# Optimization experiments

Hardware: AMD Instinct MI355X
Metric: run time of the kernel (lower is better)

The kernel has to match this reference:

```python
import jax, jax.numpy as jnp
import numpy as np

LAYERS = 20
STACKS = 2
LPS = LAYERS // STACKS  # layers per stack -> dilations 2**(l % LPS)
OUT_CH = 256
RES_CH = 64
GATE_CH = 128
SKIP_CH = 256


def setup_inputs() -> dict:
    key = jax.random.key(0)
    ks = jax.random.split(key, 16)
    B, T = 8, 16000
    s = 0.05
    inp = {
        "x": jax.random.normal(ks[0], (B, OUT_CH, T), dtype=jnp.float32),
        # first causal conv (note: original code applies w_pre to the shifted
        # input twice -> output is 2*w_pre(pre); w_cur is unused, so omitted)
        "w_pre0": jax.random.normal(ks[1], (RES_CH, OUT_CH)) * s,
        "b_pre0": jax.random.normal(ks[2], (RES_CH,)) * s,
        # per-layer dilated conv (no bias), residual block, skip projection
        "w_dil_pre": jax.random.normal(ks[3], (LAYERS, GATE_CH, RES_CH)) * s,
        "w_dil_cur": jax.random.normal(ks[4], (LAYERS, GATE_CH, RES_CH)) * s,
        "bias_h": jax.random.normal(ks[5], (LAYERS, GATE_CH)) * s,
        "w_res": jax.random.normal(ks[6], (LAYERS, RES_CH, RES_CH)) * s,
        "b_res": jax.random.normal(ks[7], (LAYERS, RES_CH)) * s,
        "w_skip": jax.random.normal(ks[8], (LAYERS, SKIP_CH, RES_CH)) * s,
        "b_skip": jax.random.normal(ks[9], (LAYERS, SKIP_CH)) * s,
        # output head
        "w_relu": jax.random.normal(ks[10], (SKIP_CH, SKIP_CH)) * s,
        "b_relu": jax.random.normal(ks[11], (SKIP_CH,)) * s,
        "w_out": jax.random.normal(ks[12], (OUT_CH, SKIP_CH)) * s,
        "b_out": jax.random.normal(ks[13], (OUT_CH,)) * s,
    }
    return inp


def _shift_right(h, d):
    # causal shift: pad d zeros on the left along time, drop last d samples
    return jnp.pad(h, ((0, 0), (0, 0), (d, 0)))[:, :, :-d]


def reference(x, w_pre0, b_pre0, w_dil_pre, w_dil_cur, bias_h,
              w_res, b_res, w_skip, b_skip, w_relu, b_relu, w_out, b_out):
    # first causal conv: original Conv2X1 'casual' path computes
    # w_pre(pre) + w_pre(pre) = 2 * w_pre(pre)  (faithful to source)
    pre = _shift_right(x, 1)
    h = 2.0 * (jnp.einsum('rc,bct->brt', w_pre0, pre) + b_pre0[None, :, None])

    skip = jnp.zeros((x.shape[0], SKIP_CH, x.shape[2]), dtype=h.dtype)
    for l in range(LAYERS):
        d = 2 ** (l % LPS)
        h_pre = _shift_right(h, d)
        # dilated 2x1 conv = two channel-wise linears (no bias), summed with bias_h
        a = (jnp.einsum('gr,brt->bgt', w_dil_pre[l], h_pre)
             + jnp.einsum('gr,brt->bgt', w_dil_cur[l], h)
             + bias_h[l][None, :, None])
        g = jnp.tanh(a[:, :RES_CH]) * jax.nn.sigmoid(a[:, RES_CH:])
        res = jnp.einsum('rq,bqt->brt', w_res[l], g) + b_res[l][None, :, None]
        h = h + res
        skip = skip + jnp.einsum('sr,brt->bst', w_skip[l], g) + b_skip[l][None, :, None]

    o = jax.nn.relu(skip)
    o = jnp.einsum('ps,bst->bpt', w_relu, o) + b_relu[None, :, None]
    o = jax.nn.relu(o)
    logits = jnp.einsum('os,bst->bot', w_out, o) + b_out[None, :, None]
    return jax.nn.softmax(logits, axis=1)  # (B, out_channels, T)
```

## Files before the change

kernel.cpp:

```cpp
#include <hip/hip_runtime.h>
#include <math.h>

#define B_ 8
#define T_ 16000
#define NBT 250
#define HROWS 16512
#define NLAY 20

typedef __attribute__((ext_vector_type(8))) short bf16x8;
typedef __attribute__((ext_vector_type(4))) float f32x4;
typedef __attribute__((ext_vector_type(4))) short sh4;

__device__ __forceinline__ unsigned short f2bf(float f){
  unsigned u = __float_as_uint(f);
  u += 0x7fffu + ((u >> 16) & 1u);
  return (unsigned short)(u >> 16);
}
__device__ __forceinline__ float bf2f(unsigned short s){
  return __uint_as_float(((unsigned)s) << 16);
}
__device__ __forceinline__ void split2(float v, unsigned short& hi, unsigned short& lo){
  hi = f2bf(v);
  lo = f2bf(v - bf2f(hi));
}

#define MFMA(a,b,c) __builtin_amdgcn_mfma_f32_16x16x32_bf16((a),(b),(c),0,0,0)

__device__ __forceinline__ void gload16(const short* gsrc, short* ldst){
  __builtin_amdgcn_global_load_lds(
      (const __attribute__((address_space(1))) unsigned int*)gsrc,
      (__attribute__((address_space(3))) unsigned int*)ldst, 16, 0, 0);
}

__global__ void k_split(const float* __restrict__ src, short* __restrict__ hi,
                        short* __restrict__ lo, int n){
  int idx = blockIdx.x * 256 + threadIdx.x;
  if (idx < n){
    unsigned short h, l; split2(src[idx], h, l);
    hi[idx] = (short)h; lo[idx] = (short)l;
  }
}
__global__ void k_split_gate(const float* __restrict__ wdp, const float* __restrict__ wdc,
                             short* __restrict__ hi, short* __restrict__ lo){
  int idx = blockIdx.x * 256 + threadIdx.x;
  if (idx < NLAY*128*128){
    int l   = idx >> 14;
    int rem = idx & 16383;
    int row = rem >> 7;
    int k   = rem & 127;
    float v = (k < 64) ? wdp[(l*128 + row)*64 + k] : wdc[(l*128 + row)*64 + (k-64)];
    unsigned short h, lo16; split2(v, h, lo16);
    hi[idx] = (short)h; lo[idx] = (short)lo16;
  }
}
__global__ void k_pack_wsf(const float* __restrict__ wsk, short* __restrict__ wsf){
  int idx = blockIdx.x * 256 + threadIdx.x;
  if (idx < NLAY*8*2*2*64*8){
    int e    = idx & 7;
    int j    = (idx >> 3) & 63;
    int kb2  = (idx >> 9) & 1;
    int half = (idx >> 10) & 1;
    int w    = (idx >> 11) & 7;
    int l    = idx >> 14;
    int row  = w*32 + half*16 + (j & 15);
    int ch   = (kb2*4 + (j >> 4))*8 + e;
    wsf[idx] = (short)f2bf(wsk[((size_t)l*256 + row)*64 + ch]);
  }
}
__global__ void k_bsum(const float* __restrict__ bsk, float* __restrict__ bsum){
  int s = threadIdx.x;
  if (s < 256){
    float a = 0.f;
#pragma unroll
    for (int l = 0; l < NLAY; ++l) a += bsk[l*256 + s];
    bsum[s] = a;
  }
}
__global__ void k_zero_guard(short* __restrict__ hA, short* __restrict__ hB){
  int idx = blockIdx.x * 256 + threadIdx.x;
  if (idx < B_*512*128){
    int b = idx / (512*128);
    int rem = idx - b*(512*128);
    size_t off = (size_t)b*HROWS*128 + rem;
    hA[off] = 0; hB[off] = 0;
  }
}

__global__ __launch_bounds__(512) void k_head_in(
    const float* __restrict__ x, const short* __restrict__ wph,
    const short* __restrict__ wpl, const float* __restrict__ bias,
    short* __restrict__ h)
{
  __shared__ short SXh[64*256], SXl[64*256];
  const int tid = threadIdx.x;
  const int bb = blockIdx.x / NBT;
  const int t0 = (blockIdx.x % NBT) * 64;
  const int lane = tid & 63, w = tid >> 6;
  const int l16 = lane & 15, l4 = lane >> 4;

  const float* xb = x + (size_t)bb * 256 * T_;
  {
    int col = lane;
    int t = t0 + col - 1;
#pragma unroll
    for (int p = 0; p < 16; ++p){
      int k0 = w*32 + p*2;
      float v0 = (t >= 0) ? xb[(size_t)k0*T_ + t] : 0.f;
      float v1 = (t >= 0) ? xb[(size_t)(k0+1)*T_ + t] : 0.f;
      unsigned short h0,l0,h1,l1; split2(v0,h0,l0); split2(v1,h1,l1);
      int idx = col*256 + (k0 ^ ((col & 15) << 3));
      ((unsigned int*)SXh)[idx>>1] = (unsigned)h0 | ((unsigned)h1 << 16);
      ((unsigned int*)SXl)[idx>>1] = (unsigned)l0 | ((unsigned)l1 << 16);
    }
  }
  __syncthreads();

  const int mi = w & 3, nh = w >> 2;
  const int rowA = mi*16 + l16;
  const int rt0 = mi*16 + l4*4;
  bf16x8 Ah[8], Al[8];
#pragma unroll
  for (int kb = 0; kb < 8; ++kb){
    int ko = kb*32 + l4*8;
    Ah[kb] = *(const bf16x8*)(wph + (size_t)rowA*256 + ko);
    Al[kb] = *(const bf16x8*)(wpl + (size_t)rowA*256 + ko);
  }
  short* hb = h + ((size_t)bb*HROWS + 512)*128;
#pragma unroll
  for (int nt = 0; nt < 2; ++nt){
    int col = (nh*2 + nt)*16 + l16;
    f32x4 acc = {0.f,0.f,0.f,0.f};
#pragma unroll
    for (int kb = 0; kb < 8; ++kb){
      int ko = (kb*32 + l4*8) ^ (l16 << 3);
      bf16x8 bhv = *(const bf16x8*)&SXh[col*256 + ko];
      bf16x8 blv = *(const bf16x8*)&SXl[col*256 + ko];
      acc = MFMA(Ah[kb], bhv, acc);
      acc = MFMA(Ah[kb], blv, acc);
      acc = MFMA(Al[kb], bhv, acc);
    }
    int t = t0 + col;
    int key = t & 15;
    int c  = rt0 >> 3, sub = rt0 & 7;
    sh4 hv, lv;
#pragma unroll
    for (int r = 0; r < 4; ++r){
      float v = 2.f*(acc[r] + bias[rt0 + r]);
      unsigned short hh, ll; split2(v, hh, ll);
      hv[r] = (short)hh; lv[r] = (short)ll;
    }
    *(sh4*)&hb[(size_t)t*128 + ((c ^ key) << 3) + sub] = hv;
    *(sh4*)&hb[(size_t)t*128 + (((c + 8) ^ key) << 3) + sub] = lv;
  }
}

__global__ __launch_bounds__(512) void k_layer4(
    const short* __restrict__ hin, short* __restrict__ hout,
    short* __restrict__ gout,
    const short* __restrict__ wgh, const short* __restrict__ wgl,
    const short* __restrict__ wrh, const short* __restrict__ wrlo,
    const float* __restrict__ bh, const float* __restrict__ br, int d)
{
  __shared__ short SH[64*128];
  __shared__ short SHP[64*128];
  __shared__ short SGh[64*64], SGl[64*64];
  const int tid = threadIdx.x;
  const int bb = blockIdx.x / NBT;
  const int tile = blockIdx.x % NBT;
  const int t0 = tile * 64;
  const int lane = tid & 63, w = tid >> 6;
  const int l16 = lane & 15, l4 = lane >> 4;

  const short* hb = hin + ((size_t)bb*HROWS + 512)*128;
  {
#pragma unroll
    for (int i = 0; i < 2; ++i){
      int colb = (w*2 + i)*4;
      const short* s1 = hb + (size_t)(t0 + colb + (lane>>4))*128 + (lane&15)*8;
      gload16(s1, &SH[colb*128]);
      const short* s2 = hb + (size_t)(t0 - d + colb + (lane>>4))*128 + (lane&15)*8;
      gload16(s2, &SHP[colb*128]);
    }
  }

  const int mi = w & 3, nh = w >> 2;
  const int rt0 = mi*16 + l4*4;
  const int rowt = mi*16 + l16, rows = 64 + mi*16 + l16;
  bf16x8 Ath[4], Atl[4], Ash[4], Asl[4];
#pragma unroll
  for (int kb = 0; kb < 4; ++kb){
    int ko = kb*32 + l4*8;
    Ath[kb] = *(const bf16x8*)(wgh + (size_t)rowt*128 + ko);
    Atl[kb] = *(const bf16x8*)(wgl + (size_t)rowt*128 + ko);
    Ash[kb] = *(const bf16x8*)(wgh + (size_t)rows*128 + ko);
    Asl[kb] = *(const bf16x8*)(wgl + (size_t)rows*128 + ko);
  }
  float bt[4], bs[4];
#pragma unroll
  for (int r = 0; r < 4; ++r){ bt[r] = bh[rt0+r]; bs[r] = bh[64+rt0+r]; }
  __syncthreads();

#pragma unroll
  for (int nt = 0; nt < 2; ++nt){
    int col = (nh*2 + nt)*16 + l16;
    int keyC = col & 15;
    int keyP = (col - d) & 15;
    f32x4 at = {0.f,0.f,0.f,0.f}, as = {0.f,0.f,0.f,0.f};
#pragma unroll
    for (int kb = 0; kb < 4; ++kb){
      const short* tile_p = (kb < 2) ? SHP : SH;
      int key = (kb < 2) ? keyP : keyC;
      int cb = (kb & 1)*4 + l4;
      bf16x8 bhv = *(const bf16x8*)&tile_p[col*128 + ((cb ^ key) << 3)];
      bf16x8 blv = *(const bf16x8*)&tile_p[col*128 + (((cb + 8) ^ key) << 3)];
      at = MFMA(Ath[kb], bhv, at);
      at = MFMA(Ath[kb], blv, at);
      at = MFMA(Atl[kb], bhv, at);
      as = MFMA(Ash[kb], bhv, as);
      as = MFMA(Ash[kb], blv, as);
      as = MFMA(Asl[kb], bhv, as);
    }
    unsigned short gh4[4], gl4[4];
#pragma unroll
    for (int r = 0; r < 4; ++r){
      float av = at[r] + bt[r];
      float sv = as[r] + bs[r];
      float e2 = __expf(2.f*av);
      float tv = 1.f - 2.f/(e2 + 1.f);
      float sg = 1.f/(1.f + __expf(-sv));
      float g  = tv*sg;
      split2(g, gh4[r], gl4[r]);
      int gi = col*64 + ((rt0 + r) ^ ((col & 7) << 3));
      SGh[gi] = (short)gh4[r]; SGl[gi] = (short)gl4[r];
    }
  }
  __syncthreads();

  {
    int f = tid >> 6, j = tid & 63;
    int row = (f >> 1)*16 + (j & 15);
    int c   = (f & 1)*4 + (j >> 4);
    bf16x8 v = *(const bf16x8*)&SGh[row*64 + ((c ^ (row & 7)) << 3)];
    *(bf16x8*)(gout + ((size_t)bb*NBT + tile)*4096 + tid*8) = v;
  }

  {
    const int rowA = mi*16 + l16;
    bf16x8 Rh[2], Rl[2];
#pragma unroll
    for (int kb = 0; kb < 2; ++kb){
      int ko = kb*32 + l4*8;
      Rh[kb] = *(const bf16x8*)(wrh  + (size_t)rowA*64 + ko);
      Rl[kb] = *(const bf16x8*)(wrlo + (size_t)rowA*64 + ko);
    }
    short* ho = hout + ((size_t)bb*HROWS + 512)*128;
    const int cH = rt0 >> 3, sub = rt0 & 7;
#pragma unroll
    for (int nt = 0; nt < 2; ++nt){
      int col = (nh*2 + nt)*16 + l16;
      int keyC = col & 15;
      f32x4 acc = {0.f,0.f,0.f,0.f};
#pragma unroll
      for (int kb = 0; kb < 2; ++kb){
        int ko = (kb*32 + l4*8) ^ ((col & 7) << 3);
        bf16x8 bhv = *(const bf16x8*)&SGh[col*64 + ko];
        bf16x8 blv = *(const bf16x8*)&SGl[col*64 + ko];
        acc = MFMA(Rh[kb], bhv, acc);
        acc = MFMA(Rh[kb], blv, acc);
        acc = MFMA(Rl[kb], bhv, acc);
      }
      sh4 hi4 = *(const sh4*)&SH[col*128 + ((cH ^ keyC) << 3) + sub];
      sh4 lo4 = *(const sh4*)&SH[col*128 + (((cH + 8) ^ keyC) << 3) + sub];
      int t = t0 + col;
      sh4 hv, lv;
#pragma unroll
      for (int r = 0; r < 4; ++r){
        float hin_f = bf2f((unsigned short)hi4[r]) + bf2f((unsigned short)lo4[r]);
        float v = hin_f + acc[r] + br[rt0 + r];
        unsigned short hh, ll; split2(v, hh, ll);
        hv[r] = (short)hh; lv[r] = (short)ll;
      }
      *(sh4*)&ho[(size_t)t*128 + ((cH ^ keyC) << 3) + sub] = hv;
      *(sh4*)&ho[(size_t)t*128 + (((cH + 8) ^ keyC) << 3) + sub] = lv;
    }
  }
}

__global__ __launch_bounds__(512) void k_head_fused(
    float* __restrict__ io,
    const short* __restrict__ g,
    const short* __restrict__ wsf,
    const float* __restrict__ bsum,
    const short* __restrict__ wrlh, const short* __restrict__ wrll,
    const float* __restrict__ brl,
    const short* __restrict__ woh, const short* __restrict__ wol,
    const float* __restrict__ bo)
{
  __shared__ short GT[2][64*64];
  __shared__ short S1h[64*256];
  const int tid = threadIdx.x;
  const int bb = blockIdx.x / NBT;
  const int tile = blockIdx.x % NBT;
  const int t0 = tile * 64;
  const int lane = tid & 63, w = tid >> 6;
  const int l16 = lane & 15, l4 = lane >> 4;

  const int r0 = w*32 + l16, r1 = w*32 + 16 + l16;
  const int rtb0 = w*32 + l4*4, rtb1 = rtb0 + 16;

  f32x4 acc0[4], acc1[4];
#pragma unroll
  for (int nt = 0; nt < 4; ++nt){ acc0[nt] = (f32x4){0.f,0.f,0.f,0.f}; acc1[nt] = (f32x4){0.f,0.f,0.f,0.f}; }

  {
    const size_t LSTR = (size_t)B_ * NBT * 4096;
    const short* gtile = g + ((size_t)bb*NBT + tile)*4096;
    const short* wb = wsf + (size_t)w*2048 + lane*8;

#define STAGE(l20, buf) gload16(gtile + (size_t)(l20)*LSTR + w*512 + lane*8, &GT[buf][w*512])

    STAGE(0, 0);
    for (int l20 = 0; l20 < 20; ++l20){
      if (l20 + 1 < 20){
        STAGE(l20 + 1, (l20 + 1) & 1);
        asm volatile("s_waitcnt vmcnt(1)" ::: "memory");
      } else {
        asm volatile("s_waitcnt vmcnt(0)" ::: "memory");
      }
      __builtin_amdgcn_s_barrier();
      __builtin_amdgcn_sched_barrier(0);
      const short* wl = wb + (size_t)l20*16384;
      bf16x8 A00 = *(const bf16x8*)(wl);
      bf16x8 A01 = *(const bf16x8*)(wl + 512);
      bf16x8 A10 = *(const bf16x8*)(wl + 1024);
      bf16x8 A11 = *(const bf16x8*)(wl + 1536);
      const short* gt = &GT[l20 & 1][0];
#pragma unroll
      for (int nt = 0; nt < 4; ++nt){
        bf16x8 B0 = *(const bf16x8*)(gt + (nt*2    )*512 + lane*8);
        bf16x8 B1 = *(const bf16x8*)(gt + (nt*2 + 1)*512 + lane*8);
        acc0[nt] = MFMA(A00, B0, acc0[nt]);
        acc0[nt] = MFMA(A01, B1, acc0[nt]);
        acc1[nt] = MFMA(A10, B0, acc1[nt]);
        acc1[nt] = MFMA(A11, B1, acc1[nt]);
      }
      __builtin_amdgcn_sched_barrier(0);
      __builtin_amdgcn_s_barrier();
    }
#undef STAGE
  }

  {
    float bs0[4], bs1[4];
#pragma unroll
    for (int r = 0; r < 4; ++r){ bs0[r] = bsum[rtb0+r]; bs1[r] = bsum[rtb1+r]; }
#pragma unroll
    for (int nt = 0; nt < 4; ++nt){
      int c2 = nt*16 + l16;
      unsigned short h[4];
#pragma unroll
      for (int r = 0; r < 4; ++r)
        h[r] = f2bf(fmaxf(acc0[nt][r] + bs0[r], 0.f));
      int i0 = c2*256 + (rtb0 ^ (l16 << 3));
      ((unsigned int*)&S1h[i0])[0] = (unsigned)h[0] | ((unsigned)h[1] << 16);
      ((unsigned int*)&S1h[i0])[1] = (unsigned)h[2] | ((unsigned)h[3] << 16);
#pragma unroll
      for (int r = 0; r < 4; ++r)
        h[r] = f2bf(fmaxf(acc1[nt][r] + bs1[r], 0.f));
      int i1 = c2*256 + (rtb1 ^ (l16 << 3));
      ((unsigned int*)&S1h[i1])[0] = (unsigned)h[0] | ((unsigned)h[1] << 16);
      ((unsigned int*)&S1h[i1])[1] = (unsigned)h[2] | ((unsigned)h[3] << 16);
    }
  }
  __syncthreads();

#pragma unroll
  for (int nt = 0; nt < 4; ++nt){ acc0[nt] = (f32x4){0.f,0.f,0.f,0.f}; acc1[nt] = (f32x4){0.f,0.f,0.f,0.f}; }
#pragma unroll
  for (int kb = 0; kb < 8; ++kb){
    int ko = kb*32 + l4*8;
    bf16x8 A0h = *(const bf16x8*)(wrlh + (size_t)r0*256 + ko);
    bf16x8 A0l = *(const bf16x8*)(wrll + (size_t)r0*256 + ko);
    bf16x8 A1h = *(const bf16x8*)(wrlh + (size_t)r1*256 + ko);
    bf16x8 A1l = *(const bf16x8*)(wrll + (size_t)r1*256 + ko);
#pragma unroll
    for (int nt = 0; nt < 4; ++nt){
      int c2 = nt*16 + l16;
      int kos = ko ^ (l16 << 3);
      bf16x8 bhv = *(const bf16x8*)&S1h[c2*256 + kos];
      acc0[nt] = MFMA(A0h, bhv, acc0[nt]);
      acc0[nt] = MFMA(A0l, bhv, acc0[nt]);
      acc1[nt] = MFMA(A1h, bhv, acc1[nt]);
      acc1[nt] = MFMA(A1l, bhv, acc1[nt]);
    }
  }
  __syncthreads();
  {
    float br0[4], br1[4];
#pragma unroll
    for (int r = 0; r < 4; ++r){ br0[r] = brl[rtb0+r]; br1[r] = brl[rtb1+r]; }
#pragma unroll
    for (int nt = 0; nt < 4; ++nt){
      int c2 = nt*16 + l16;
      unsigned short h[4];
#pragma unroll
      for (int r = 0; r < 4; ++r)
        h[r] = f2bf(fmaxf(acc0[nt][r] + br0[r], 0.f));
      int i0 = c2*256 + (rtb0 ^ (l16 << 3));
      ((unsigned int*)&S1h[i0])[0] = (unsigned)h[0] | ((unsigned)h[1] << 16);
      ((unsigned int*)&S1h[i0])[1] = (unsigned)h[2] | ((unsigned)h[3] << 16);
#pragma unroll
      for (int r = 0; r < 4; ++r)
        h[r] = f2bf(fmaxf(acc1[nt][r] + br1[r], 0.f));
      int i1 = c2*256 + (rtb1 ^ (l16 << 3));
      ((unsigned int*)&S1h[i1])[0] = (unsigned)h[0] | ((unsigned)h[1] << 16);
      ((unsigned int*)&S1h[i1])[1] = (unsigned)h[2] | ((unsigned)h[3] << 16);
    }
  }
  __syncthreads();

#pragma unroll
  for (int nt = 0; nt < 4; ++nt){ acc0[nt] = (f32x4){0.f,0.f,0.f,0.f}; acc1[nt] = (f32x4){0.f,0.f,0.f,0.f}; }
#pragma unroll
  for (int kb = 0; kb < 8; ++kb){
    int ko = kb*32 + l4*8;
    bf16x8 A0h = *(const bf16x8*)(woh + (size_t)r0*256 + ko);
    bf16x8 A0l = *(const bf16x8*)(wol + (size_t)r0*256 + ko);
    bf16x8 A1h = *(const bf16x8*)(woh + (size_t)r1*256 + ko);
    bf16x8 A1l = *(const bf16x8*)(wol + (size_t)r1*256 + ko);
#pragma unroll
    for (int nt = 0; nt < 4; ++nt){
      int c2 = nt*16 + l16;
      int kos = ko ^ (l16 << 3);
      bf16x8 bhv = *(const bf16x8*)&S1h[c2*256 + kos];
      acc0[nt] = MFMA(A0h, bhv, acc0[nt]);
      acc0[nt] = MFMA(A0l, bhv, acc0[nt]);
      acc1[nt] = MFMA(A1h, bhv, acc1[nt]);
      acc1[nt] = MFMA(A1l, bhv, acc1[nt]);
    }
  }
  float* smax = (float*)&GT[0][0];
  float* ssum = smax + 512;
  float* iob = io + (size_t)bb * 256 * T_;
  float bo0[4], bo1[4];
#pragma unroll
  for (int r = 0; r < 4; ++r){ bo0[r] = bo[rtb0+r]; bo1[r] = bo[rtb1+r]; }
#pragma unroll
  for (int nt = 0; nt < 4; ++nt){
    float m = -1e30f;
#pragma unroll
    for (int r = 0; r < 4; ++r){
      acc0[nt][r] += bo0[r];
      acc1[nt][r] += bo1[r];
      m = fmaxf(m, fmaxf(acc0[nt][r], acc1[nt][r]));
    }
    m = fmaxf(m, __shfl_xor(m, 16, 64));
    m = fmaxf(m, __shfl_xor(m, 32, 64));
    smax[w*64 + nt*16 + l16] = m;
  }
  __syncthreads();
#pragma unroll
  for (int nt = 0; nt < 4; ++nt){
    float m = smax[nt*16 + l16];
#pragma unroll
    for (int ww = 1; ww < 8; ++ww) m = fmaxf(m, smax[ww*64 + nt*16 + l16]);
    float s = 0.f;
#pragma unroll
    for (int r = 0; r < 4; ++r){
      acc0[nt][r] = __expf(acc0[nt][r] - m); s += acc0[nt][r];
      acc1[nt][r] = __expf(acc1[nt][r] - m); s += acc1[nt][r];
    }
    s += __shfl_xor(s, 16, 64);
    s += __shfl_xor(s, 32, 64);
    ssum[w*64 + nt*16 + l16] = s;
  }
  __syncthreads();
#pragma unroll
  for (int nt = 0; nt < 4; ++nt){
    float S = 0.f;
#pragma unroll
    for (int ww = 0; ww < 8; ++ww) S += ssum[ww*64 + nt*16 + l16];
    float inv = 1.f / S;
    int t = t0 + nt*16 + l16;
#pragma unroll
    for (int r = 0; r < 4; ++r){
      iob[(size_t)(rtb0 + r)*T_ + t] = acc0[nt][r]*inv;
      iob[(size_t)(rtb1 + r)*T_ + t] = acc1[nt][r]*inv;
    }
  }
}

extern "C" void kernel_launch(void* const* d_in, const int* in_sizes, int n_in,
                              void* d_out, int out_size, void* d_ws, size_t ws_size,
                              hipStream_t stream) {
  const float* x       = (const float*)d_in[0];
  const float* w_pre0  = (const float*)d_in[1];
  const float* b_pre0  = (const float*)d_in[2];
  const float* w_dil_p = (const float*)d_in[3];
  const float* w_dil_c = (const float*)d_in[4];
  const float* bias_h  = (const float*)d_in[5];
  const float* w_res   = (const float*)d_in[6];
  const float* b_res   = (const float*)d_in[7];
  const float* w_skip  = (const float*)d_in[8];
  const float* b_skip  = (const float*)d_in[9];
  const float* w_relu  = (const float*)d_in[10];
  const float* b_relu  = (const float*)d_in[11];
  const float* w_out   = (const float*)d_in[12];
  const float* b_out   = (const float*)d_in[13];

  float* out = (float*)d_out;
  short* hA = (short*)d_ws;
  short* hB = hA + (size_t)B_ * HROWS * 128;
  float* bsum = (float*)(hB + (size_t)B_ * HROWS * 128);
  short* p   = (short*)(bsum + 256);
  short* WPh = p; p += 16384;  short* WPl = p; p += 16384;
  short* WGh = p; p += 327680; short* WGl = p; p += 327680;
  short* WRh = p; p += 81920;  short* WRl = p; p += 81920;
  short* WSF = p; p += 327680;
  short* WLh = p; p += 65536;  short* WLl = p; p += 65536;
  short* WOh = p; p += 65536;  short* WOl = p; p += 65536;
  short* GBUF = p;

  k_split<<<64, 256, 0, stream>>>(w_pre0, WPh, WPl, 16384);
  k_split_gate<<<1280, 256, 0, stream>>>(w_dil_p, w_dil_c, WGh, WGl);
  k_split<<<320, 256, 0, stream>>>(w_res, WRh, WRl, 81920);
  k_pack_wsf<<<1280, 256, 0, stream>>>(w_skip, WSF);
  k_split<<<256, 256, 0, stream>>>(w_relu, WLh, WLl, 65536);
  k_split<<<256, 256, 0, stream>>>(w_out, WOh, WOl, 65536);
  k_zero_guard<<<2048, 256, 0, stream>>>(hA, hB);
  k_bsum<<<1, 256, 0, stream>>>(b_skip, bsum);

  k_head_in<<<B_ * NBT, 512, 0, stream>>>(x, WPh, WPl, b_pre0, hA);

  const short* hin = hA;
  short* houtp = hB;
  for (int l = 0; l < NLAY; ++l) {
    int d = 1 << (l % 10);
    k_layer4<<<B_ * NBT, 512, 0, stream>>>(
        hin, houtp,
        GBUF + (size_t)l * B_ * NBT * 4096,
        WGh + (size_t)l*16384, WGl + (size_t)l*16384,
        WRh + (size_t)l*4096,  WRl + (size_t)l*4096,
        bias_h + (size_t)l*128, b_res + (size_t)l*64, d);
    const short* tmp = hin;
    hin = houtp;
    houtp = (short*)tmp;
  }

  k_head_fused<<<B_ * NBT, 512, 0, stream>>>(
      out, GBUF, WSF, bsum, WLh, WLl, b_relu, WOh, WOl, b_out);
}
```

Before: 1.333 ms.

## Make layer kernel persistent over four tiles with double-buffered prefetch

The per-layer kernel now processes four consecutive time tiles per block, loading the gate and residual weights once and double-buffering the next tile's current and shifted h rows into LDS while the current tile computes. The separate shifted tile is merged into one 128-row window, reusing overlapping rows when the dilation is below 64. The head kernel aliases its LDS buffers into one pool and issues the skip-weight loads before the barrier. The aims are lower weight-reload and load-latency cost and higher occupancy, at the price of four times fewer blocks and extra barriers.

```diff
diff --git a/kernel.cpp b/kernel.cpp
--- a/kernel.cpp
+++ b/kernel.cpp
@@ -154,37 +154,23 @@
   }
 }
 
-__global__ __launch_bounds__(512) void k_layer4(
+__global__ __launch_bounds__(512, 4) void k_layer5(
     const short* __restrict__ hin, short* __restrict__ hout,
     short* __restrict__ gout,
     const short* __restrict__ wgh, const short* __restrict__ wgl,
     const short* __restrict__ wrh, const short* __restrict__ wrlo,
     const float* __restrict__ bh, const float* __restrict__ br, int d)
 {
-  __shared__ short SH[64*128];
-  __shared__ short SHP[64*128];
+  __shared__ short SHX[2][128*128];
   __shared__ short SGh[64*64], SGl[64*64];
   const int tid = threadIdx.x;
-  const int bb = blockIdx.x / NBT;
-  const int tile = blockIdx.x % NBT;
-  const int t0 = tile * 64;
   const int lane = tid & 63, w = tid >> 6;
   const int l16 = lane & 15, l4 = lane >> 4;
-
-  const short* hb = hin + ((size_t)bb*HROWS + 512)*128;
-  {
-#pragma unroll
-    for (int i = 0; i < 2; ++i){
-      int colb = (w*2 + i)*4;
-      const short* s1 = hb + (size_t)(t0 + colb + (lane>>4))*128 + (lane&15)*8;
-      gload16(s1, &SH[colb*128]);
-      const short* s2 = hb + (size_t)(t0 - d + colb + (lane>>4))*128 + (lane&15)*8;
-      gload16(s2, &SHP[colb*128]);
-    }
-  }
-
   const int mi = w & 3, nh = w >> 2;
   const int rt0 = mi*16 + l4*4;
+  const int dmax = (d > 64) ? d : 64;
+  const int spoff = (d < 64) ? (64 - d) : 0;
+
   const int rowt = mi*16 + l16, rows = 64 + mi*16 + l16;
   bf16x8 Ath[4], Atl[4], Ash[4], Asl[4];
 #pragma unroll
@@ -195,94 +181,130 @@
     Ash[kb] = *(const bf16x8*)(wgh + (size_t)rows*128 + ko);
     Asl[kb] = *(const bf16x8*)(wgl + (size_t)rows*128 + ko);
   }
-  float bt[4], bs[4];
-#pragma unroll
-  for (int r = 0; r < 4; ++r){ bt[r] = bh[rt0+r]; bs[r] = bh[64+rt0+r]; }
-  __syncthreads();
-
-#pragma unroll
-  for (int nt = 0; nt < 2; ++nt){
-    int col = (nh*2 + nt)*16 + l16;
-    int keyC = col & 15;
-    int keyP = (col - d) & 15;
-    f32x4 at = {0.f,0.f,0.f,0.f}, as = {0.f,0.f,0.f,0.f};
-#pragma unroll
-    for (int kb = 0; kb < 4; ++kb){
-      const short* tile_p = (kb < 2) ? SHP : SH;
-      int key = (kb < 2) ? keyP : keyC;
-      int cb = (kb & 1)*4 + l4;
-      bf16x8 bhv = *(const bf16x8*)&tile_p[col*128 + ((cb ^ key) << 3)];
-      bf16x8 blv = *(const bf16x8*)&tile_p[col*128 + (((cb + 8) ^ key) << 3)];
-      at = MFMA(Ath[kb], bhv, at);
-      at = MFMA(Ath[kb], blv, at);
-      at = MFMA(Atl[kb], bhv, at);
-      as = MFMA(Ash[kb], bhv, as);
-      as = MFMA(Ash[kb], blv, as);
-      as = MFMA(Asl[kb], bhv, as);
-    }
-    unsigned short gh4[4], gl4[4];
-#pragma unroll
-    for (int r = 0; r < 4; ++r){
-      float av = at[r] + bt[r];
-      float sv = as[r] + bs[r];
-      float e2 = __expf(2.f*av);
-      float tv = 1.f - 2.f/(e2 + 1.f);
-      float sg = 1.f/(1.f + __expf(-sv));
-      float g  = tv*sg;
-      split2(g, gh4[r], gl4[r]);
-      int gi = col*64 + ((rt0 + r) ^ ((col & 7) << 3));
-      SGh[gi] = (short)gh4[r]; SGl[gi] = (short)gl4[r];
-    }
-  }
-  __syncthreads();
-
-  {
-    int f = tid >> 6, j = tid & 63;
-    int row = (f >> 1)*16 + (j & 15);
-    int c   = (f & 1)*4 + (j >> 4);
-    bf16x8 v = *(const bf16x8*)&SGh[row*64 + ((c ^ (row & 7)) << 3)];
-    *(bf16x8*)(gout + ((size_t)bb*NBT + tile)*4096 + tid*8) = v;
-  }
-
-  {
-    const int rowA = mi*16 + l16;
-    bf16x8 Rh[2], Rl[2];
-#pragma unroll
-    for (int kb = 0; kb < 2; ++kb){
-      int ko = kb*32 + l4*8;
-      Rh[kb] = *(const bf16x8*)(wrh  + (size_t)rowA*64 + ko);
-      Rl[kb] = *(const bf16x8*)(wrlo + (size_t)rowA*64 + ko);
-    }
-    short* ho = hout + ((size_t)bb*HROWS + 512)*128;
-    const int cH = rt0 >> 3, sub = rt0 & 7;
+  bf16x8 Rh[2], Rl[2];
+#pragma unroll
+  for (int kb = 0; kb < 2; ++kb){
+    int ko = kb*32 + l4*8;
+    Rh[kb] = *(const bf16x8*)(wrh  + (size_t)rowt*64 + ko);
+    Rl[kb] = *(const bf16x8*)(wrlo + (size_t)rowt*64 + ko);
+  }
+  float bt[4], bs[4], brv[4];
+#pragma unroll
+  for (int r = 0; r < 4; ++r){
+    bt[r] = bh[rt0+r]; bs[r] = bh[64+rt0+r]; brv[r] = br[rt0+r];
+  }
+
+  const int gt0 = blockIdx.x * 4;
+
+  auto STAGE = [&](int gt, int buf){
+    int bb2 = gt / NBT;
+    int t0s = (gt % NBT) * 64;
+    const short* hb2 = hin + ((size_t)bb2*HROWS + 512)*128;
+#pragma unroll
+    for (int j = 0; j < 4; ++j){
+      int chunk = j >> 1;
+      int rq = (w*2 + (j & 1))*4;
+      int grow = (chunk ? t0s : t0s - dmax) + rq + (lane >> 4);
+      gload16(hb2 + (size_t)grow*128 + (lane & 15)*8,
+              &SHX[buf][(chunk*64 + rq)*128]);
+    }
+  };
+
+  STAGE(gt0, 0);
+  for (int it = 0; it < 4; ++it){
+    const int gt = gt0 + it;
+    const int bb = gt / NBT, tile = gt % NBT;
+    const int t0 = tile * 64;
+    if (it < 3){
+      STAGE(gt + 1, (it + 1) & 1);
+      asm volatile("s_waitcnt vmcnt(4)" ::: "memory");
+    } else {
+      asm volatile("s_waitcnt vmcnt(0)" ::: "memory");
+    }
+    __builtin_amdgcn_s_barrier();
+    __builtin_amdgcn_sched_barrier(0);
+
+    const short* SX = &SHX[it & 1][0];
 #pragma unroll
     for (int nt = 0; nt < 2; ++nt){
       int col = (nh*2 + nt)*16 + l16;
-      int keyC = col & 15;
-      f32x4 acc = {0.f,0.f,0.f,0.f};
-#pragma unroll
-      for (int kb = 0; kb < 2; ++kb){
-        int ko = (kb*32 + l4*8) ^ ((col & 7) << 3);
-        bf16x8 bhv = *(const bf16x8*)&SGh[col*64 + ko];
-        bf16x8 blv = *(const bf16x8*)&SGl[col*64 + ko];
-        acc = MFMA(Rh[kb], bhv, acc);
-        acc = MFMA(Rh[kb], blv, acc);
-        acc = MFMA(Rl[kb], bhv, acc);
+      int keyC = (t0 + col) & 15;
+      int keyP = (t0 + col - d) & 15;
+      f32x4 at = {0.f,0.f,0.f,0.f}, as = {0.f,0.f,0.f,0.f};
+#pragma unroll
+      for (int kb = 0; kb < 4; ++kb){
+        int xr  = (kb < 2) ? (spoff + col) : (64 + col);
+        int key = (kb < 2) ? keyP : keyC;
+        int cb = (kb & 1)*4 + l4;
+        bf16x8 bhv = *(const bf16x8*)&SX[xr*128 + ((cb ^ key) << 3)];
+        bf16x8 blv = *(const bf16x8*)&SX[xr*128 + (((cb + 8) ^ key) << 3)];
+        at = MFMA(Ath[kb], bhv, at);
+        at = MFMA(Ath[kb], blv, at);
+        at = MFMA(Atl[kb], bhv, at);
+        as = MFMA(Ash[kb], bhv, as);
+        as = MFMA(Ash[kb], blv, as);
+        as = MFMA(Asl[kb], bhv, as);
       }
-      sh4 hi4 = *(const sh4*)&SH[col*128 + ((cH ^ keyC) << 3) + sub];
-      sh4 lo4 = *(const sh4*)&SH[col*128 + (((cH + 8) ^ keyC) << 3) + sub];
-      int t = t0 + col;
-      sh4 hv, lv;
+      unsigned short gh4[4], gl4[4];
 #pragma unroll
       for (int r = 0; r < 4; ++r){
-        float hin_f = bf2f((unsigned short)hi4[r]) + bf2f((unsigned short)lo4[r]);
-        float v = hin_f + acc[r] + br[rt0 + r];
-        unsigned short hh, ll; split2(v, hh, ll);
-        hv[r] = (short)hh; lv[r] = (short)ll;
+        float av = at[r] + bt[r];
+        float sv = as[r] + bs[r];
+        float e2 = __expf(2.f*av);
+        float tv = 1.f - 2.f/(e2 + 1.f);
+        float sg = 1.f/(1.f + __expf(-sv));
+        float g  = tv*sg;
+        split2(g, gh4[r], gl4[r]);
+        int gi = col*64 + ((rt0 + r) ^ ((col & 7) << 3));
+        SGh[gi] = (short)gh4[r]; SGl[gi] = (short)gl4[r];
       }
-      *(sh4*)&ho[(size_t)t*128 + ((cH ^ keyC) << 3) + sub] = hv;
-      *(sh4*)&ho[(size_t)t*128 + (((cH + 8) ^ keyC) << 3) + sub] = lv;
-    }
+    }
+    asm volatile("s_waitcnt lgkmcnt(0)" ::: "memory");
+    __builtin_amdgcn_sched_barrier(0);
+    __builtin_amdgcn_s_barrier();
+
+    {
+      int f = tid >> 6, j = tid & 63;
+      int row = (f >> 1)*16 + (j & 15);
+      int c   = (f & 1)*4 + (j >> 4);
+      bf16x8 v = *(const bf16x8*)&SGh[row*64 + ((c ^ (row & 7)) << 3)];
+      *(bf16x8*)(gout + ((size_t)bb*NBT + tile)*4096 + tid*8) = v;
+    }
+
+    {
+      short* ho = hout + ((size_t)bb*HROWS + 512)*128;
+      const int cH = rt0 >> 3, sub = rt0 & 7;
+#pragma unroll
+      for (int nt = 0; nt < 2; ++nt){
+        int col = (nh*2 + nt)*16 + l16;
+        int keyC = (t0 + col) & 15;
+        f32x4 acc = {0.f,0.f,0.f,0.f};
+#pragma unroll
+        for (int kb = 0; kb < 2; ++kb){
+          int ko = (kb*32 + l4*8) ^ ((col & 7) << 3);
+          bf16x8 bhv = *(const bf16x8*)&SGh[col*64 + ko];
+          bf16x8 blv = *(const bf16x8*)&SGl[col*64 + ko];
+          acc = MFMA(Rh[kb], bhv, acc);
+          acc = MFMA(Rh[kb], blv, acc);
+          acc = MFMA(Rl[kb], bhv, acc);
+        }
+        sh4 hi4 = *(const sh4*)&SX[(64 + col)*128 + ((cH ^ keyC) << 3) + sub];
+        sh4 lo4 = *(const sh4*)&SX[(64 + col)*128 + (((cH + 8) ^ keyC) << 3) + sub];
+        int t = t0 + col;
+        sh4 hv, lv;
+#pragma unroll
+        for (int r = 0; r < 4; ++r){
+          float hin_f = bf2f((unsigned short)hi4[r]) + bf2f((unsigned short)lo4[r]);
+          float v = hin_f + acc[r] + brv[r];
+          unsigned short hh, ll; split2(v, hh, ll);
+          hv[r] = (short)hh; lv[r] = (short)ll;
+        }
+        *(sh4*)&ho[(size_t)t*128 + ((cH ^ keyC) << 3) + sub] = hv;
+        *(sh4*)&ho[(size_t)t*128 + (((cH + 8) ^ keyC) << 3) + sub] = lv;
+      }
+    }
+    __builtin_amdgcn_sched_barrier(0);
+    __builtin_amdgcn_s_barrier();
   }
 }
 
@@ -296,8 +318,7 @@
     const short* __restrict__ woh, const short* __restrict__ wol,
     const float* __restrict__ bo)
 {
-  __shared__ short GT[2][64*64];
-  __shared__ short S1h[64*256];
+  __shared__ short POOL[16384];
   const int tid = threadIdx.x;
   const int bb = blockIdx.x / NBT;
   const int tile = blockIdx.x % NBT;
@@ -317,10 +338,15 @@
     const short* gtile = g + ((size_t)bb*NBT + tile)*4096;
     const short* wb = wsf + (size_t)w*2048 + lane*8;
 
-#define STAGE(l20, buf) gload16(gtile + (size_t)(l20)*LSTR + w*512 + lane*8, &GT[buf][w*512])
+#define STAGE(l20, buf) gload16(gtile + (size_t)(l20)*LSTR + w*512 + lane*8, &POOL[(buf)*4096 + w*512])
 
     STAGE(0, 0);
     for (int l20 = 0; l20 < 20; ++l20){
+      const short* wl = wb + (size_t)l20*16384;
+      bf16x8 A00 = *(const bf16x8*)(wl);
+      bf16x8 A01 = *(const bf16x8*)(wl + 512);
+      bf16x8 A10 = *(const bf16x8*)(wl + 1024);
+      bf16x8 A11 = *(const bf16x8*)(wl + 1536);
       if (l20 + 1 < 20){
         STAGE(l20 + 1, (l20 + 1) & 1);
         asm volatile("s_waitcnt vmcnt(1)" ::: "memory");
@@ -329,12 +355,7 @@
       }
       __builtin_amdgcn_s_barrier();
       __builtin_amdgcn_sched_barrier(0);
-      const short* wl = wb + (size_t)l20*16384;
-      bf16x8 A00 = *(const bf16x8*)(wl);
-      bf16x8 A01 = *(const bf16x8*)(wl + 512);
-      bf16x8 A10 = *(const bf16x8*)(wl + 1024);
-      bf16x8 A11 = *(const bf16x8*)(wl + 1536);
-      const short* gt = &GT[l20 & 1][0];
+      const short* gt = &POOL[(l20 & 1)*4096];
 #pragma unroll
       for (int nt = 0; nt < 4; ++nt){
         bf16x8 B0 = *(const bf16x8*)(gt + (nt*2    )*512 + lane*8);
@@ -350,6 +371,7 @@
 #undef STAGE
   }
 
+  short* S1h = POOL;
   {
     float bs0[4], bs1[4];
 #pragma unroll
@@ -439,7 +461,8 @@
       acc1[nt] = MFMA(A1l, bhv, acc1[nt]);
     }
   }
-  float* smax = (float*)&GT[0][0];
+  __syncthreads();
+  float* smax = (float*)POOL;
   float* ssum = smax + 512;
   float* iob = io + (size_t)bb * 256 * T_;
   float bo0[4], bo1[4];
@@ -536,7 +559,7 @@
   short* houtp = hB;
   for (int l = 0; l < NLAY; ++l) {
     int d = 1 << (l % 10);
-    k_layer4<<<B_ * NBT, 512, 0, stream>>>(
+    k_layer5<<<B_ * NBT / 4, 512, 0, stream>>>(
         hin, houtp,
         GBUF + (size_t)l * B_ * NBT * 4096,
         WGh + (size_t)l*16384, WGl + (size_t)l*16384,
```

Measured after the change: 1.982 ms. +48.7%, slower.

## Add small-dilation layer kernel reusing tile rows for shifted input; merge head shared buffers

Applied to the files above, without the earlier changes.

Adds a specialized layer kernel for dilations up to 32. It loads the 64-column h tile once and reads the shifted (pre) rows from the same shared tile, fetching only a small prefix of d columns from global memory. The goal is to cut the duplicate global reads of the shifted input that the generic layer kernel does. Separately, the head kernel folds its shared buffers into one pool to lower LDS use, and issues the per-layer weight loads before the barrier so they overlap the staging wait; this adds an extra __syncthreads.

```diff
diff --git a/kernel.cpp b/kernel.cpp
--- a/kernel.cpp
+++ b/kernel.cpp
@@ -286,6 +286,143 @@
   }
 }
 
+__global__ __launch_bounds__(512) void k_layer_sd(
+    const short* __restrict__ hin, short* __restrict__ hout,
+    short* __restrict__ gout,
+    const short* __restrict__ wgh, const short* __restrict__ wgl,
+    const short* __restrict__ wrh, const short* __restrict__ wrlo,
+    const float* __restrict__ bh, const float* __restrict__ br, int d)
+{
+  __shared__ short SH[64*128];
+  __shared__ short PREF[32*128];
+  __shared__ short SGh[64*64], SGl[64*64];
+  const int tid = threadIdx.x;
+  const int bb = blockIdx.x / NBT;
+  const int tile = blockIdx.x % NBT;
+  const int t0 = tile * 64;
+  const int lane = tid & 63, w = tid >> 6;
+  const int l16 = lane & 15, l4 = lane >> 4;
+
+  const short* hb = hin + ((size_t)bb*HROWS + 512)*128;
+  {
+#pragma unroll
+    for (int i = 0; i < 2; ++i){
+      int colb = (w*2 + i)*4;
+      const short* s1 = hb + (size_t)(t0 + colb + (lane>>4))*128 + (lane&15)*8;
+      gload16(s1, &SH[colb*128]);
+    }
+    if (w*4 < d){
+      const short* s2 = hb + (size_t)(t0 - d + w*4 + (lane>>4))*128 + (lane&15)*8;
+      gload16(s2, &PREF[(w*4)*128]);
+    }
+  }
+
+  const int mi = w & 3, nh = w >> 2;
+  const int rt0 = mi*16 + l4*4;
+  const int rowt = mi*16 + l16, rows = 64 + mi*16 + l16;
+  bf16x8 Ath[4], Atl[4], Ash[4], Asl[4];
+#pragma unroll
+  for (int kb = 0; kb < 4; ++kb){
+    int ko = kb*32 + l4*8;
+    Ath[kb] = *(const bf16x8*)(wgh + (size_t)rowt*128 + ko);
+    Atl[kb] = *(const bf16x8*)(wgl + (size_t)rowt*128 + ko);
+    Ash[kb] = *(const bf16x8*)(wgh + (size_t)rows*128 + ko);
+    Asl[kb] = *(const bf16x8*)(wgl + (size_t)rows*128 + ko);
+  }
+  float bt[4], bs[4];
+#pragma unroll
+  for (int r = 0; r < 4; ++r){ bt[r] = bh[rt0+r]; bs[r] = bh[64+rt0+r]; }
+  __syncthreads();
+
+#pragma unroll
+  for (int nt = 0; nt < 2; ++nt){
+    int col = (nh*2 + nt)*16 + l16;
+    int keyC = col & 15;
+    int keyP = (col - d) & 15;
+    int colp = col - d;
+    const short* prow = (colp >= 0) ? &SH[colp*128] : &PREF[col*128];
+    const short* crow = &SH[col*128];
+    f32x4 at = {0.f,0.f,0.f,0.f}, as = {0.f,0.f,0.f,0.f};
+#pragma unroll
+    for (int kb = 0; kb < 4; ++kb){
+      const short* base = (kb < 2) ? prow : crow;
+      int key = (kb < 2) ? keyP : keyC;
+      int cb = (kb & 1)*4 + l4;
+      bf16x8 bhv = *(const bf16x8*)&base[((cb ^ key) << 3)];
+      bf16x8 blv = *(const bf16x8*)&base[(((cb + 8) ^ key) << 3)];
+      at = MFMA(Ath[kb], bhv, at);
+      at = MFMA(Ath[kb], blv, at);
+      at = MFMA(Atl[kb], bhv, at);
+      as = MFMA(Ash[kb], bhv, as);
+      as = MFMA(Ash[kb], blv, as);
+      as = MFMA(Asl[kb], bhv, as);
+    }
+    unsigned short gh4[4], gl4[4];
+#pragma unroll
+    for (int r = 0; r < 4; ++r){
+      float av = at[r] + bt[r];
+      float sv = as[r] + bs[r];
+      float e2 = __expf(2.f*av);
+      float tv = 1.f - 2.f/(e2 + 1.f);
+      float sg = 1.f/(1.f + __expf(-sv));
+      float g  = tv*sg;
+      split2(g, gh4[r], gl4[r]);
+      int gi = col*64 + ((rt0 + r) ^ ((col & 7) << 3));
+      SGh[gi] = (short)gh4[r]; SGl[gi] = (short)gl4[r];
+    }
+  }
+  __syncthreads();
+
+  {
+    int f = tid >> 6, j = tid & 63;
+    int row = (f >> 1)*16 + (j & 15);
+    int c   = (f & 1)*4 + (j >> 4);
+    bf16x8 v = *(const bf16x8*)&SGh[row*64 + ((c ^ (row & 7)) << 3)];
+    *(bf16x8*)(gout + ((size_t)bb*NBT + tile)*4096 + tid*8) = v;
+  }
+
+  {
+    const int rowA = mi*16 + l16;
+    bf16x8 Rh[2], Rl[2];
+#pragma unroll
+    for (int kb = 0; kb < 2; ++kb){
+      int ko = kb*32 + l4*8;
+      Rh[kb] = *(const bf16x8*)(wrh  + (size_t)rowA*64 + ko);
+      Rl[kb] = *(const bf16x8*)(wrlo + (size_t)rowA*64 + ko);
+    }
+    short* ho = hout + ((size_t)bb*HROWS + 512)*128;
+    const int cH = rt0 >> 3, sub = rt0 & 7;
+#pragma unroll
+    for (int nt = 0; nt < 2; ++nt){
+      int col = (nh*2 + nt)*16 + l16;
+      int keyC = col & 15;
+      f32x4 acc = {0.f,0.f,0.f,0.f};
+#pragma unroll
+      for (int kb = 0; kb < 2; ++kb){
+        int ko = (kb*32 + l4*8) ^ ((col & 7) << 3);
+        bf16x8 bhv = *(const bf16x8*)&SGh[col*64 + ko];
+        bf16x8 blv = *(const bf16x8*)&SGl[col*64 + ko];
+        acc = MFMA(Rh[kb], bhv, acc);
+        acc = MFMA(Rh[kb], blv, acc);
+        acc = MFMA(Rl[kb], bhv, acc);
+      }
+      sh4 hi4 = *(const sh4*)&SH[col*128 + ((cH ^ keyC) << 3) + sub];
+      sh4 lo4 = *(const sh4*)&SH[col*128 + (((cH + 8) ^ keyC) << 3) + sub];
+      int t = t0 + col;
+      sh4 hv, lv;
+#pragma unroll
+      for (int r = 0; r < 4; ++r){
+        float hin_f = bf2f((unsigned short)hi4[r]) + bf2f((unsigned short)lo4[r]);
+        float v = hin_f + acc[r] + br[rt0 + r];
+        unsigned short hh, ll; split2(v, hh, ll);
+        hv[r] = (short)hh; lv[r] = (short)ll;
+      }
+      *(sh4*)&ho[(size_t)t*128 + ((cH ^ keyC) << 3) + sub] = hv;
+      *(sh4*)&ho[(size_t)t*128 + (((cH + 8) ^ keyC) << 3) + sub] = lv;
+    }
+  }
+}
+
 __global__ __launch_bounds__(512) void k_head_fused(
     float* __restrict__ io,
     const short* __restrict__ g,
@@ -296,8 +433,7 @@
     const short* __restrict__ woh, const short* __restrict__ wol,
     const float* __restrict__ bo)
 {
-  __shared__ short GT[2][64*64];
-  __shared__ short S1h[64*256];
+  __shared__ short POOL[16384];
   const int tid = threadIdx.x;
   const int bb = blockIdx.x / NBT;
   const int tile = blockIdx.x % NBT;
@@ -317,10 +453,15 @@
     const short* gtile = g + ((size_t)bb*NBT + tile)*4096;
     const short* wb = wsf + (size_t)w*2048 + lane*8;
 
-#define STAGE(l20, buf) gload16(gtile + (size_t)(l20)*LSTR + w*512 + lane*8, &GT[buf][w*512])
+#define STAGE(l20, buf) gload16(gtile + (size_t)(l20)*LSTR + w*512 + lane*8, &POOL[(buf)*4096 + w*512])
 
     STAGE(0, 0);
     for (int l20 = 0; l20 < 20; ++l20){
+      const short* wl = wb + (size_t)l20*16384;
+      bf16x8 A00 = *(const bf16x8*)(wl);
+      bf16x8 A01 = *(const bf16x8*)(wl + 512);
+      bf16x8 A10 = *(const bf16x8*)(wl + 1024);
+      bf16x8 A11 = *(const bf16x8*)(wl + 1536);
       if (l20 + 1 < 20){
         STAGE(l20 + 1, (l20 + 1) & 1);
         asm volatile("s_waitcnt vmcnt(1)" ::: "memory");
@@ -329,12 +470,7 @@
       }
       __builtin_amdgcn_s_barrier();
       __builtin_amdgcn_sched_barrier(0);
-      const short* wl = wb + (size_t)l20*16384;
-      bf16x8 A00 = *(const bf16x8*)(wl);
-      bf16x8 A01 = *(const bf16x8*)(wl + 512);
-      bf16x8 A10 = *(const bf16x8*)(wl + 1024);
-      bf16x8 A11 = *(const bf16x8*)(wl + 1536);
-      const short* gt = &GT[l20 & 1][0];
+      const short* gt = &POOL[(l20 & 1)*4096];
 #pragma unroll
       for (int nt = 0; nt < 4; ++nt){
         bf16x8 B0 = *(const bf16x8*)(gt + (nt*2    )*512 + lane*8);
@@ -350,6 +486,7 @@
 #undef STAGE
   }
 
+  short* S1h = POOL;
   {
     float bs0[4], bs1[4];
 #pragma unroll
@@ -439,7 +576,8 @@
       acc1[nt] = MFMA(A1l, bhv, acc1[nt]);
     }
   }
-  float* smax = (float*)&GT[0][0];
+  __syncthreads();
+  float* smax = (float*)POOL;
   float* ssum = smax + 512;
   float* iob = io + (size_t)bb * 256 * T_;
   float bo0[4], bo1[4];
@@ -536,12 +674,21 @@
   short* houtp = hB;
   for (int l = 0; l < NLAY; ++l) {
     int d = 1 << (l % 10);
-    k_layer4<<<B_ * NBT, 512, 0, stream>>>(
-        hin, houtp,
-        GBUF + (size_t)l * B_ * NBT * 4096,
-        WGh + (size_t)l*16384, WGl + (size_t)l*16384,
-        WRh + (size_t)l*4096,  WRl + (size_t)l*4096,
-        bias_h + (size_t)l*128, b_res + (size_t)l*64, d);
+    if (d <= 32) {
+      k_layer_sd<<<B_ * NBT, 512, 0, stream>>>(
+          hin, houtp,
+          GBUF + (size_t)l * B_ * NBT * 4096,
+          WGh + (size_t)l*16384, WGl + (size_t)l*16384,
+          WRh + (size_t)l*4096,  WRl + (size_t)l*4096,
+          bias_h + (size_t)l*128, b_res + (size_t)l*64, d);
+    } else {
+      k_layer4<<<B_ * NBT, 512, 0, stream>>>(
+          hin, houtp,
+          GBUF + (size_t)l * B_ * NBT * 4096,
+          WGh + (size_t)l*16384, WGl + (size_t)l*16384,
+          WRh + (size_t)l*4096,  WRl + (size_t)l*4096,
+          bias_h + (size_t)l*128, b_res + (size_t)l*64, d);
+    }
     const short* tmp = hin;
     hin = houtp;
     houtp = (short*)tmp;
```

After: 1.340 ms. About the same (+0.5%).

## Cut LDS and register use in layer and head kernels to raise occupancy

Applied to the files above, without the earlier changes.

The layer kernel drops its separate gate LDS buffers and reuses the previous-tap tile buffer after a barrier. It streams gate weights per k-block instead of keeping all 16 fragments in registers, and sets launch bounds to 6 blocks per CU. The head kernel merges its LDS arrays into one pool, shrinking shared memory from 48KB to 32KB, and issues the skip-weight loads before the stage wait. The aim is more resident blocks per CU to hide latency, at the cost of extra barriers and possible register pressure or spills under the tighter bound.

```diff
diff --git a/kernel.cpp b/kernel.cpp
--- a/kernel.cpp
+++ b/kernel.cpp
@@ -154,7 +154,7 @@
   }
 }
 
-__global__ __launch_bounds__(512) void k_layer4(
+__global__ __launch_bounds__(512, 6) void k_layer6(
     const short* __restrict__ hin, short* __restrict__ hout,
     short* __restrict__ gout,
     const short* __restrict__ wgh, const short* __restrict__ wgl,
@@ -163,7 +163,6 @@
 {
   __shared__ short SH[64*128];
   __shared__ short SHP[64*128];
-  __shared__ short SGh[64*64], SGl[64*64];
   const int tid = threadIdx.x;
   const int bb = blockIdx.x / NBT;
   const int tile = blockIdx.x % NBT;
@@ -186,53 +185,95 @@
   const int mi = w & 3, nh = w >> 2;
   const int rt0 = mi*16 + l4*4;
   const int rowt = mi*16 + l16, rows = 64 + mi*16 + l16;
-  bf16x8 Ath[4], Atl[4], Ash[4], Asl[4];
-#pragma unroll
-  for (int kb = 0; kb < 4; ++kb){
-    int ko = kb*32 + l4*8;
-    Ath[kb] = *(const bf16x8*)(wgh + (size_t)rowt*128 + ko);
-    Atl[kb] = *(const bf16x8*)(wgl + (size_t)rowt*128 + ko);
-    Ash[kb] = *(const bf16x8*)(wgh + (size_t)rows*128 + ko);
-    Asl[kb] = *(const bf16x8*)(wgl + (size_t)rows*128 + ko);
-  }
   float bt[4], bs[4];
 #pragma unroll
   for (int r = 0; r < 4; ++r){ bt[r] = bh[rt0+r]; bs[r] = bh[64+rt0+r]; }
   __syncthreads();
 
+  f32x4 at0 = {0.f,0.f,0.f,0.f}, at1 = {0.f,0.f,0.f,0.f};
+  f32x4 as0 = {0.f,0.f,0.f,0.f}, as1 = {0.f,0.f,0.f,0.f};
+  {
+#pragma unroll
+    for (int kb = 0; kb < 2; ++kb){
+      int ko = kb*32 + l4*8;
+      bf16x8 Wth = *(const bf16x8*)(wgh + (size_t)rowt*128 + ko);
+      bf16x8 Wtl = *(const bf16x8*)(wgl + (size_t)rowt*128 + ko);
+      bf16x8 Wsh = *(const bf16x8*)(wgh + (size_t)rows*128 + ko);
+      bf16x8 Wsl = *(const bf16x8*)(wgl + (size_t)rows*128 + ko);
+      int cb = kb*4 + l4;
+#pragma unroll
+      for (int nt = 0; nt < 2; ++nt){
+        int col = (nh*2 + nt)*16 + l16;
+        int keyP = (col - d) & 15;
+        bf16x8 bhv = *(const bf16x8*)&SHP[col*128 + ((cb ^ keyP) << 3)];
+        bf16x8 blv = *(const bf16x8*)&SHP[col*128 + (((cb + 8) ^ keyP) << 3)];
+        if (nt == 0){
+          at0 = MFMA(Wth, bhv, at0); at0 = MFMA(Wth, blv, at0); at0 = MFMA(Wtl, bhv, at0);
+          as0 = MFMA(Wsh, bhv, as0); as0 = MFMA(Wsh, blv, as0); as0 = MFMA(Wsl, bhv, as0);
+        } else {
+          at1 = MFMA(Wth, bhv, at1); at1 = MFMA(Wth, blv, at1); at1 = MFMA(Wtl, bhv, at1);
+          as1 = MFMA(Wsh, bhv, as1); as1 = MFMA(Wsh, blv, as1); as1 = MFMA(Wsl, bhv, as1);
+        }
+      }
+    }
+  }
+  {
+#pragma unroll
+    for (int kb = 2; kb < 4; ++kb){
+      int ko = kb*32 + l4*8;
+      bf16x8 Wth = *(const bf16x8*)(wgh + (size_t)rowt*128 + ko);
+      bf16x8 Wtl = *(const bf16x8*)(wgl + (size_t)rowt*128 + ko);
+      bf16x8 Wsh = *(const bf16x8*)(wgh + (size_t)rows*128 + ko);
+      bf16x8 Wsl = *(const bf16x8*)(wgl + (size_t)rows*128 + ko);
+      int cb = (kb & 1)*4 + l4;
+#pragma unroll
+      for (int nt = 0; nt < 2; ++nt){
+        int col = (nh*2 + nt)*16 + l16;
+        int keyC = col & 15;
+        bf16x8 bhv = *(const bf16x8*)&SH[col*128 + ((cb ^ keyC) << 3)];
+        bf16x8 blv = *(const bf16x8*)&SH[col*128 + (((cb + 8) ^ keyC) << 3)];
+        if (nt == 0){
+          at0 = MFMA(Wth, bhv, at0); at0 = MFMA(Wth, blv, at0); at0 = MFMA(Wtl, bhv, at0);
+          as0 = MFMA(Wsh, bhv, as0); as0 = MFMA(Wsh, blv, as0); as0 = MFMA(Wsl, bhv, as0);
+        } else {
+          at1 = MFMA(Wth, bhv, at1); at1 = MFMA(Wth, blv, at1); at1 = MFMA(Wtl, bhv, at1);
+          as1 = MFMA(Wsh, bhv, as1); as1 = MFMA(Wsh, blv, as1); as1 = MFMA(Wsl, bhv, as1);
+        }
+      }
+    }
+  }
+
+  unsigned gp[2][4];
 #pragma unroll
   for (int nt = 0; nt < 2; ++nt){
-    int col = (nh*2 + nt)*16 + l16;
-    int keyC = col & 15;
-    int keyP = (col - d) & 15;
-    f32x4 at = {0.f,0.f,0.f,0.f}, as = {0.f,0.f,0.f,0.f};
-#pragma unroll
-    for (int kb = 0; kb < 4; ++kb){
-      const short* tile_p = (kb < 2) ? SHP : SH;
-      int key = (kb < 2) ? keyP : keyC;
-      int cb = (kb & 1)*4 + l4;
-      bf16x8 bhv = *(const bf16x8*)&tile_p[col*128 + ((cb ^ key) << 3)];
-      bf16x8 blv = *(const bf16x8*)&tile_p[col*128 + (((cb + 8) ^ key) << 3)];
-      at = MFMA(Ath[kb], bhv, at);
-      at = MFMA(Ath[kb], blv, at);
-      at = MFMA(Atl[kb], bhv, at);
-      as = MFMA(Ash[kb], bhv, as);
-      as = MFMA(Ash[kb], blv, as);
-      as = MFMA(Asl[kb], bhv, as);
-    }
     unsigned short gh4[4], gl4[4];
 #pragma unroll
     for (int r = 0; r < 4; ++r){
-      float av = at[r] + bt[r];
-      float sv = as[r] + bs[r];
+      float av = ((nt == 0) ? at0[r] : at1[r]) + bt[r];
+      float sv = ((nt == 0) ? as0[r] : as1[r]) + bs[r];
       float e2 = __expf(2.f*av);
       float tv = 1.f - 2.f/(e2 + 1.f);
       float sg = 1.f/(1.f + __expf(-sv));
       float g  = tv*sg;
       split2(g, gh4[r], gl4[r]);
-      int gi = col*64 + ((rt0 + r) ^ ((col & 7) << 3));
-      SGh[gi] = (short)gh4[r]; SGl[gi] = (short)gl4[r];
-    }
+    }
+    gp[nt][0] = (unsigned)gh4[0] | ((unsigned)gh4[1] << 16);
+    gp[nt][1] = (unsigned)gh4[2] | ((unsigned)gh4[3] << 16);
+    gp[nt][2] = (unsigned)gl4[0] | ((unsigned)gl4[1] << 16);
+    gp[nt][3] = (unsigned)gl4[2] | ((unsigned)gl4[3] << 16);
+  }
+  __syncthreads();
+
+  short* SGh = SHP;
+  short* SGl = SHP + 4096;
+#pragma unroll
+  for (int nt = 0; nt < 2; ++nt){
+    int col = (nh*2 + nt)*16 + l16;
+    int gib = col*64 + (rt0 ^ ((col & 7) << 3));
+    ((unsigned int*)&SGh[gib])[0] = gp[nt][0];
+    ((unsigned int*)&SGh[gib])[1] = gp[nt][1];
+    ((unsigned int*)&SGl[gib])[0] = gp[nt][2];
+    ((unsigned int*)&SGl[gib])[1] = gp[nt][3];
   }
   __syncthreads();
 
@@ -296,8 +337,7 @@
     const short* __restrict__ woh, const short* __restrict__ wol,
     const float* __restrict__ bo)
 {
-  __shared__ short GT[2][64*64];
-  __shared__ short S1h[64*256];
+  __shared__ short POOL[16384];
   const int tid = threadIdx.x;
   const int bb = blockIdx.x / NBT;
   const int tile = blockIdx.x % NBT;
@@ -317,10 +357,15 @@
     const short* gtile = g + ((size_t)bb*NBT + tile)*4096;
     const short* wb = wsf + (size_t)w*2048 + lane*8;
 
-#define STAGE(l20, buf) gload16(gtile + (size_t)(l20)*LSTR + w*512 + lane*8, &GT[buf][w*512])
+#define STAGE(l20, buf) gload16(gtile + (size_t)(l20)*LSTR + w*512 + lane*8, &POOL[(buf)*4096 + w*512])
 
     STAGE(0, 0);
     for (int l20 = 0; l20 < 20; ++l20){
+      const short* wl = wb + (size_t)l20*16384;
+      bf16x8 A00 = *(const bf16x8*)(wl);
+      bf16x8 A01 = *(const bf16x8*)(wl + 512);
+      bf16x8 A10 = *(const bf16x8*)(wl + 1024);
+      bf16x8 A11 = *(const bf16x8*)(wl + 1536);
       if (l20 + 1 < 20){
         STAGE(l20 + 1, (l20 + 1) & 1);
         asm volatile("s_waitcnt vmcnt(1)" ::: "memory");
@@ -329,12 +374,7 @@
       }
       __builtin_amdgcn_s_barrier();
       __builtin_amdgcn_sched_barrier(0);
-      const short* wl = wb + (size_t)l20*16384;
-      bf16x8 A00 = *(const bf16x8*)(wl);
-      bf16x8 A01 = *(const bf16x8*)(wl + 512);
-      bf16x8 A10 = *(const bf16x8*)(wl + 1024);
-      bf16x8 A11 = *(const bf16x8*)(wl + 1536);
-      const short* gt = &GT[l20 & 1][0];
+      const short* gt = &POOL[(l20 & 1)*4096];
 #pragma unroll
       for (int nt = 0; nt < 4; ++nt){
         bf16x8 B0 = *(const bf16x8*)(gt + (nt*2    )*512 + lane*8);
@@ -350,6 +390,7 @@
 #undef STAGE
   }
 
+  short* S1h = POOL;
   {
     float bs0[4], bs1[4];
 #pragma unroll
@@ -439,7 +480,8 @@
       acc1[nt] = MFMA(A1l, bhv, acc1[nt]);
     }
   }
-  float* smax = (float*)&GT[0][0];
+  __syncthreads();
+  float* smax = (float*)POOL;
   float* ssum = smax + 512;
   float* iob = io + (size_t)bb * 256 * T_;
   float bo0[4], bo1[4];
@@ -536,7 +578,7 @@
   short* houtp = hB;
   for (int l = 0; l < NLAY; ++l) {
     int d = 1 << (l % 10);
-    k_layer4<<<B_ * NBT, 512, 0, stream>>>(
+    k_layer6<<<B_ * NBT, 512, 0, stream>>>(
         hin, houtp,
         GBUF + (size_t)l * B_ * NBT * 4096,
         WGh + (size_t)l*16384, WGl + (size_t)l*16384,
```

Measured after the change: 1.328 ms (median of 2 runs). Within noise of the previous version (-0.4%).
